# Kernel optimization log

Hardware: AMD Instinct MI355X
Metric: run time of the kernel (lower is better)

The kernel has to match this reference:

```python
import jax, jax.numpy as jnp
import numpy as np


def setup_inputs() -> dict:
    key0 = jax.random.key(0)
    kq, kk, kv, kl = jax.random.split(key0, 4)
    B, L, V, D = 2, 512, 64, 128
    N_CLUSTERS = 8
    return {
        "query": jax.random.normal(kq, (B, L, V, D), dtype=jnp.float32),
        "key": jax.random.normal(kk, (B, L, V, D), dtype=jnp.float32),
        "value": jax.random.normal(kv, (B, L, V, D), dtype=jnp.float32),
        "label_arr": jax.random.randint(kl, (B, L), 0, N_CLUSTERS, dtype=jnp.int64)
        if jax.config.jax_enable_x64
        else jax.random.randint(kl, (B, L), 0, N_CLUSTERS, dtype=jnp.int32),
    }


def reference(query, key, value, label_arr):
    # query/key/value: (b, l, v, d); label_arr: (b, l)
    b, l, v, d = query.shape
    scale = 1.0 / (d ** 0.5)  # self.scale defaults to 1/sqrt(d_model)

    # sum of key over the v (cluster-member) dimension -> (b, l, d)
    sum_tot_vec = key.sum(axis=2)

    # scores[b,i,k,j] = query[b,i,k,:] . sum_tot_vec[b,j,:]
    scores = jnp.einsum("bikd,bjd->bikj", query, sum_tot_vec)

    # label-based mask: positions attend only within the same cluster label
    label_mask = label_arr[:, :, None] == label_arr[:, None, :]  # (b, l, l)
    scores = jnp.where(label_mask[:, :, None, :], scores, -jnp.inf)

    # masked softmax over the last (j) axis; every row has >=1 valid entry (self)
    A = jax.nn.softmax(scale * scores, axis=-1)

    # V[b,i,k,d] = sum_j A[b,i,k,j] * value[b,j,k,d]
    out = jnp.einsum("bikj,bjkd->bikd", A, value)
    return out
```

## Files before the change

kernel.cpp:

```cpp
#include <hip/hip_runtime.h>
#include <math.h>

#define B_ 2
#define L_ 512
#define V_ 64
#define D_ 128
#define NC_ 8
#define NMAX 128
#define PSTR 136
#define SCALE 0.08838834764831845f

#define FB_THREADS 128
#define FB_IT 64
#define FB_JT 8
#define MAXIT (L_ / FB_IT)

typedef short s16x8 __attribute__((ext_vector_type(8)));
typedef float f32x4 __attribute__((ext_vector_type(4)));

__device__ __forceinline__ unsigned short f2bf(float x) {
  unsigned int u = __float_as_uint(x);
  u += 0x7FFFu + ((u >> 16) & 1u);
  return (unsigned short)(u >> 16);
}
__device__ __forceinline__ float bf2f(unsigned short h) {
  return __uint_as_float((unsigned int)h << 16);
}

__global__ __launch_bounds__(L_) void cluster_index_kernel(
    const int* __restrict__ label, int* __restrict__ counts, int* __restrict__ jlist) {
  int b = blockIdx.x;
  int tid = threadIdx.x;
  __shared__ int lab[L_];
  lab[tid] = label[b * L_ + tid];
  if (tid < NC_) counts[b * NC_ + tid] = 0;
  __syncthreads();
  int my = lab[tid];
  int rank = 0, cnt = 0;
  for (int j = 0; j < L_; ++j) {
    int e = (lab[j] == my) ? 1 : 0;
    cnt += e;
    if (j < tid) rank += e;
  }
  jlist[(b * NC_ + my) * L_ + rank] = tid;
  if (rank == 0) counts[b * NC_ + my] = cnt;
}

__global__ __launch_bounds__(256) void sumkey_kernel(
    const float* __restrict__ key, float* __restrict__ S,
    unsigned short* __restrict__ Sh, unsigned short* __restrict__ Sl) {
  int idx = blockIdx.x * 256 + threadIdx.x;
  int d4 = idx & 31;
  int bj = idx >> 5;
  const float4* kp = (const float4*)(key + (size_t)bj * V_ * D_) + d4;
  float4 s = make_float4(0.f, 0.f, 0.f, 0.f);
#pragma unroll 8
  for (int v = 0; v < V_; ++v) {
    float4 x = kp[v * 32];
    s.x += x.x; s.y += x.y; s.z += x.z; s.w += x.w;
  }
  *((float4*)S + idx) = s;
  unsigned short h0 = f2bf(s.x), h1 = f2bf(s.y), h2 = f2bf(s.z), h3 = f2bf(s.w);
  *((ushort4*)Sh + idx) = make_ushort4(h0, h1, h2, h3);
  *((ushort4*)Sl + idx) = make_ushort4(
      f2bf(s.x - bf2f(h0)), f2bf(s.y - bf2f(h1)),
      f2bf(s.z - bf2f(h2)), f2bf(s.w - bf2f(h3)));
}

__global__ __launch_bounds__(256, 2) void fused_attn_kernel(
    const float* __restrict__ q, const float* __restrict__ vg,
    const unsigned short* __restrict__ Sh, const unsigned short* __restrict__ Sl,
    const int* __restrict__ counts, const int* __restrict__ jlist,
    float* __restrict__ out) {
  int bid = blockIdx.x;
  int k = bid & (V_ - 1);
  int c = (bid >> 6) & (NC_ - 1);
  int b = bid >> 9;
  int bc = b * NC_ + c;
  int n = counts[bc];
  if (n == 0 || n > NMAX) return;
  int np32 = (n + 31) & ~31;
  int nt = np32 >> 4;
  int ktn = np32 >> 5;
  int mtn = (n + 15) >> 4;

  int tid = threadIdx.x;
  int w = tid >> 6;
  int l = tid & 63, lr = l & 15, lg = l >> 4;

  __shared__ int jl[NMAX];
  __shared__ __align__(16) unsigned short VTh[64][PSTR];
  __shared__ __align__(16) unsigned short VTl[64][PSTR];
  __shared__ __align__(16) unsigned short Pm[NMAX][PSTR];

  for (int j = tid; j < np32; j += 256) jl[j] = jlist[bc * L_ + min(j, n - 1)];
  __syncthreads();

  auto stage_vt = [&](int dbase) {
    int d4 = tid & 15, jj = tid >> 4;
    for (int j = jj; j < np32; j += 16) {
      float4 x = *(const float4*)(vg + ((size_t)(b * L_ + jl[j]) * V_ + k) * D_
                                  + dbase + d4 * 4);
      float xs[4] = {x.x, x.y, x.z, x.w};
#pragma unroll
      for (int e = 0; e < 4; ++e) {
        unsigned short h = f2bf(xs[e]);
        VTh[d4 * 4 + e][j] = h;
        VTl[d4 * 4 + e][j] = f2bf(xs[e] - bf2f(h));
      }
    }
  };

  auto pv_half = [&](int dbase) {
    for (int mt = w; mt < mtn; mt += 4) {
#pragma unroll
      for (int dt = 0; dt < 4; ++dt) {
        f32x4 o = {0.f, 0.f, 0.f, 0.f};
#pragma unroll
        for (int kt = 0; kt < 4; ++kt) {
          if (kt < ktn) {
            s16x8 pa = *(const s16x8*)&Pm[mt * 16 + lr][kt * 32 + lg * 8];
            s16x8 vh = *(const s16x8*)&VTh[dt * 16 + lr][kt * 32 + lg * 8];
            s16x8 vl = *(const s16x8*)&VTl[dt * 16 + lr][kt * 32 + lg * 8];
            o = __builtin_amdgcn_mfma_f32_16x16x32_bf16(pa, vh, o, 0, 0, 0);
            o = __builtin_amdgcn_mfma_f32_16x16x32_bf16(pa, vl, o, 0, 0, 0);
          }
        }
#pragma unroll
        for (int reg = 0; reg < 4; ++reg) {
          int i = mt * 16 + lg * 4 + reg;
          if (i < n)
            out[((size_t)(b * L_ + jl[i]) * V_ + k) * D_ + dbase + dt * 16 + lr]
                = o[reg];
        }
      }
    }
  };

  stage_vt(0);
  __syncthreads();

  for (int mt = w; mt < mtn; mt += 4) {
    const float* qb = q + ((size_t)(b * L_ + jl[mt * 16 + lr]) * V_ + k) * D_ + lg * 8;
    s16x8 Ah[4], Al[4];
#pragma unroll
    for (int kk = 0; kk < 4; ++kk) {
      float4 x0 = *(const float4*)(qb + kk * 32);
      float4 x1 = *(const float4*)(qb + kk * 32 + 4);
      float xs[8] = {x0.x, x0.y, x0.z, x0.w, x1.x, x1.y, x1.z, x1.w};
#pragma unroll
      for (int e = 0; e < 8; ++e) {
        unsigned short h = f2bf(xs[e]);
        Ah[kk][e] = (short)h;
        Al[kk][e] = (short)f2bf(xs[e] - bf2f(h));
      }
    }

    f32x4 acc[8];
#pragma unroll
    for (int jt = 0; jt < 8; ++jt) {
      if (jt < nt) {
        int jrow = jl[jt * 16 + lr];
        const unsigned short* sbh = Sh + (size_t)(b * L_ + jrow) * D_ + lg * 8;
        const unsigned short* sbl = Sl + (size_t)(b * L_ + jrow) * D_ + lg * 8;
        f32x4 a = {0.f, 0.f, 0.f, 0.f};
#pragma unroll
        for (int kk = 0; kk < 4; ++kk) {
          s16x8 bh = *(const s16x8*)(sbh + kk * 32);
          s16x8 bl = *(const s16x8*)(sbl + kk * 32);
          a = __builtin_amdgcn_mfma_f32_16x16x32_bf16(Ah[kk], bh, a, 0, 0, 0);
          a = __builtin_amdgcn_mfma_f32_16x16x32_bf16(Al[kk], bh, a, 0, 0, 0);
          a = __builtin_amdgcn_mfma_f32_16x16x32_bf16(Ah[kk], bl, a, 0, 0, 0);
        }
        acc[jt] = a;
      }
    }

#pragma unroll
    for (int reg = 0; reg < 4; ++reg) {
      float sv[8];
      float mx = -3.0e38f;
#pragma unroll
      for (int jt = 0; jt < 8; ++jt) {
        if (jt < nt) {
          float x = ((jt * 16 + lr) < n) ? acc[jt][reg] * SCALE : -3.0e38f;
          sv[jt] = x;
          mx = fmaxf(mx, x);
        }
      }
      mx = fmaxf(mx, __shfl_xor(mx, 1));
      mx = fmaxf(mx, __shfl_xor(mx, 2));
      mx = fmaxf(mx, __shfl_xor(mx, 4));
      mx = fmaxf(mx, __shfl_xor(mx, 8));
      float sum = 0.f;
#pragma unroll
      for (int jt = 0; jt < 8; ++jt) {
        if (jt < nt) {
          float p = __expf(sv[jt] - mx);
          p = ((jt * 16 + lr) < n) ? p : 0.f;
          sv[jt] = p;
          sum += p;
        }
      }
      sum += __shfl_xor(sum, 1);
      sum += __shfl_xor(sum, 2);
      sum += __shfl_xor(sum, 4);
      sum += __shfl_xor(sum, 8);
      float inv = 1.0f / sum;
      int prow = mt * 16 + lg * 4 + reg;
#pragma unroll
      for (int jt = 0; jt < 8; ++jt)
        if (jt < nt) Pm[prow][jt * 16 + lr] = f2bf(sv[jt] * inv);
    }
  }

  pv_half(0);
  __syncthreads();
  stage_vt(64);
  __syncthreads();
  pv_half(64);
}

__global__ __launch_bounds__(FB_THREADS, 2) void clustered_attn_kernel(
    const float* __restrict__ q, const float* __restrict__ value,
    const float* __restrict__ S, const int* __restrict__ counts,
    const int* __restrict__ jlist, float* __restrict__ out) {
  int bid = blockIdx.x;
  int k = bid & (V_ - 1);
  int c = (bid >> 6) & (NC_ - 1);
  int b = (bid >> 9) & (B_ - 1);
  int itile = bid >> 10;
  int bc = b * NC_ + c;
  int n = counts[bc];
  if (n <= NMAX) return;
  int it0 = itile * FB_IT;
  if (it0 >= n) return;

  int tid = threadIdx.x;
  int dh = tid & 7;
  int sl = tid >> 3;

  __shared__ int jl[L_];
  __shared__ float S_t[FB_JT][D_];
  __shared__ float V_t[FB_JT][D_];

  for (int j = tid; j < n; j += FB_THREADS) jl[j] = jlist[bc * L_ + j];
  __syncthreads();

  bool act[4];
  float4 q4[4][4];
#pragma unroll
  for (int r = 0; r < 4; ++r) {
    int row = it0 + sl + 16 * r;
    act[r] = row < n;
    int i = jl[act[r] ? row : it0];
    const float* qrow = q + (size_t)((b * L_ + i) * V_ + k) * D_;
#pragma unroll
    for (int t = 0; t < 4; ++t) q4[r][t] = *(const float4*)(qrow + (dh + 8 * t) * 4);
  }

  float4 acc4[4][4];
#pragma unroll
  for (int r = 0; r < 4; ++r)
#pragma unroll
    for (int t = 0; t < 4; ++t) acc4[r][t] = make_float4(0.f, 0.f, 0.f, 0.f);
  float m[4], lden[4];
#pragma unroll
  for (int r = 0; r < 4; ++r) { m[r] = -INFINITY; lden[r] = 0.f; }

  const float4* S_t4 = (const float4*)&S_t[0][0];
  const float4* V_t4 = (const float4*)&V_t[0][0];

  for (int jt0 = 0; jt0 < n; jt0 += FB_JT) {
    int jn = min(FB_JT, n - jt0);
    __syncthreads();
#pragma unroll
    for (int rep = 0; rep < 2; ++rep) {
      int idx = tid + rep * FB_THREADS;
      int jj = idx >> 5;
      int d4 = idx & 31;
      int j = jl[jt0 + min(jj, jn - 1)];
      size_t rowbase = (size_t)(b * L_ + j);
      ((float4*)&S_t[0][0])[idx] = *(const float4*)(S + rowbase * D_ + d4 * 4);
      ((float4*)&V_t[0][0])[idx] =
          *(const float4*)(value + (rowbase * V_ + k) * D_ + d4 * 4);
    }
    __syncthreads();

    float s[4][FB_JT];
#pragma unroll
    for (int r = 0; r < 4; ++r)
#pragma unroll
      for (int jj = 0; jj < FB_JT; ++jj) s[r][jj] = 0.f;
#pragma unroll
    for (int t = 0; t < 4; ++t) {
#pragma unroll
      for (int jj = 0; jj < FB_JT; ++jj) {
        float4 sv = S_t4[jj * 32 + dh + 8 * t];
#pragma unroll
        for (int r = 0; r < 4; ++r) {
          float4 qv = q4[r][t];
          s[r][jj] = fmaf(qv.x, sv.x,
                     fmaf(qv.y, sv.y, fmaf(qv.z, sv.z, fmaf(qv.w, sv.w, s[r][jj]))));
        }
      }
    }
#pragma unroll
    for (int r = 0; r < 4; ++r)
#pragma unroll
      for (int jj = 0; jj < FB_JT; ++jj) {
        float v = s[r][jj] + __shfl_xor(s[r][jj], 1);
        v += __shfl_xor(v, 2);
        v += __shfl_xor(v, 4);
        s[r][jj] = v * SCALE;
      }
#pragma unroll
    for (int r = 0; r < 4; ++r) {
      float mnew = m[r];
#pragma unroll
      for (int jj = 0; jj < FB_JT; ++jj)
        if (jj < jn) mnew = fmaxf(mnew, s[r][jj]);
      float f = __expf(m[r] - mnew);
      m[r] = mnew;
#pragma unroll
      for (int t = 0; t < 4; ++t) {
        acc4[r][t].x *= f; acc4[r][t].y *= f;
        acc4[r][t].z *= f; acc4[r][t].w *= f;
      }
      float sum = 0.f;
#pragma unroll
      for (int jj = 0; jj < FB_JT; ++jj) {
        float p = (jj < jn) ? __expf(s[r][jj] - mnew) : 0.f;
        s[r][jj] = p;
        sum += p;
      }
      lden[r] = lden[r] * f + sum;
    }
#pragma unroll
    for (int t = 0; t < 4; ++t) {
#pragma unroll
      for (int jj = 0; jj < FB_JT; ++jj) {
        float4 vv = V_t4[jj * 32 + dh + 8 * t];
#pragma unroll
        for (int r = 0; r < 4; ++r) {
          float p = s[r][jj];
          acc4[r][t].x = fmaf(p, vv.x, acc4[r][t].x);
          acc4[r][t].y = fmaf(p, vv.y, acc4[r][t].y);
          acc4[r][t].z = fmaf(p, vv.z, acc4[r][t].z);
          acc4[r][t].w = fmaf(p, vv.w, acc4[r][t].w);
        }
      }
    }
  }

#pragma unroll
  for (int r = 0; r < 4; ++r) {
    if (act[r]) {
      int i = jl[it0 + sl + 16 * r];
      float inv = 1.0f / lden[r];
      float* op = out + (size_t)((b * L_ + i) * V_ + k) * D_;
#pragma unroll
      for (int t = 0; t < 4; ++t) {
        float4 o;
        o.x = acc4[r][t].x * inv;
        o.y = acc4[r][t].y * inv;
        o.z = acc4[r][t].z * inv;
        o.w = acc4[r][t].w * inv;
        *(float4*)(op + (dh + 8 * t) * 4) = o;
      }
    }
  }
}

extern "C" void kernel_launch(void* const* d_in, const int* in_sizes, int n_in,
                              void* d_out, int out_size, void* d_ws, size_t ws_size,
                              hipStream_t stream) {
  const float* q = (const float*)d_in[0];
  const float* key = (const float*)d_in[1];
  const float* value = (const float*)d_in[2];
  const int* label = (const int*)d_in[3];
  float* out = (float*)d_out;

  char* w8 = (char*)d_ws;
  int* counts = (int*)(w8 + 0);
  int* jlist = (int*)(w8 + 256);
  float* S = (float*)(w8 + 33280);
  unsigned short* Sh = (unsigned short*)(w8 + 557568);
  unsigned short* Sl = (unsigned short*)(w8 + 819712);

  cluster_index_kernel<<<B_, L_, 0, stream>>>(label, counts, jlist);
  sumkey_kernel<<<(B_ * L_ * D_ / 4) / 256, 256, 0, stream>>>(key, S, Sh, Sl);
  fused_attn_kernel<<<B_ * NC_ * V_, 256, 0, stream>>>(
      q, value, Sh, Sl, counts, jlist, out);
  clustered_attn_kernel<<<B_ * NC_ * V_ * MAXIT, FB_THREADS, 0, stream>>>(
      q, value, S, counts, jlist, out);
}
```

Baseline: 202.5 us.

## Stream value chunks with online softmax and cluster-contiguous summed keys

The fused attention kernel now processes keys in 32-wide chunks with an online (flash-style) softmax. This shrinks shared memory so four blocks can fit per CU, and the grid is split into two query-row halves per (batch, cluster, head). The summed-key bf16 hi/lo arrays are written in cluster-sorted order using new position and base arrays, so score loads are contiguous instead of gathered. The sum-key kernel is reorganized to one block per row with a shared-memory reduction. The trade-off is that each value chunk is staged and converted redundantly by both half-blocks, and there are more barriers per chunk.

```diff
diff --git a/kernel.cpp b/kernel.cpp
--- a/kernel.cpp
+++ b/kernel.cpp
@@ -7,7 +7,7 @@
 #define D_ 128
 #define NC_ 8
 #define NMAX 128
-#define PSTR 136
+#define VSTR 40
 #define SCALE 0.08838834764831845f
 
 #define FB_THREADS 128
@@ -28,7 +28,8 @@
 }
 
 __global__ __launch_bounds__(L_) void cluster_index_kernel(
-    const int* __restrict__ label, int* __restrict__ counts, int* __restrict__ jlist) {
+    const int* __restrict__ label, int* __restrict__ counts,
+    int* __restrict__ jlist, int* __restrict__ posarr, int* __restrict__ bases) {
   int b = blockIdx.x;
   int tid = threadIdx.x;
   __shared__ int lab[L_];
@@ -36,113 +37,78 @@
   if (tid < NC_) counts[b * NC_ + tid] = 0;
   __syncthreads();
   int my = lab[tid];
-  int rank = 0, cnt = 0;
+  int rank = 0, cnt = 0, base = 0;
   for (int j = 0; j < L_; ++j) {
     int e = (lab[j] == my) ? 1 : 0;
     cnt += e;
     if (j < tid) rank += e;
+    if (lab[j] < my) base++;
   }
   jlist[(b * NC_ + my) * L_ + rank] = tid;
-  if (rank == 0) counts[b * NC_ + my] = cnt;
+  posarr[b * L_ + tid] = base + rank;
+  if (rank == 0) { counts[b * NC_ + my] = cnt; bases[b * NC_ + my] = base; }
 }
 
 __global__ __launch_bounds__(256) void sumkey_kernel(
-    const float* __restrict__ key, float* __restrict__ S,
-    unsigned short* __restrict__ Sh, unsigned short* __restrict__ Sl) {
-  int idx = blockIdx.x * 256 + threadIdx.x;
-  int d4 = idx & 31;
-  int bj = idx >> 5;
-  const float4* kp = (const float4*)(key + (size_t)bj * V_ * D_) + d4;
-  float4 s = make_float4(0.f, 0.f, 0.f, 0.f);
+    const float* __restrict__ key, const int* __restrict__ posarr,
+    float* __restrict__ S, unsigned short* __restrict__ Sch,
+    unsigned short* __restrict__ Scl) {
+  int bj = blockIdx.x;
+  int tid = threadIdx.x;
+  int d = tid & 127, vh = tid >> 7;
+  const float* kp = key + (size_t)bj * V_ * D_ + vh * 32 * D_ + d;
+  float s = 0.f;
 #pragma unroll 8
-  for (int v = 0; v < V_; ++v) {
-    float4 x = kp[v * 32];
-    s.x += x.x; s.y += x.y; s.z += x.z; s.w += x.w;
-  }
-  *((float4*)S + idx) = s;
-  unsigned short h0 = f2bf(s.x), h1 = f2bf(s.y), h2 = f2bf(s.z), h3 = f2bf(s.w);
-  *((ushort4*)Sh + idx) = make_ushort4(h0, h1, h2, h3);
-  *((ushort4*)Sl + idx) = make_ushort4(
-      f2bf(s.x - bf2f(h0)), f2bf(s.y - bf2f(h1)),
-      f2bf(s.z - bf2f(h2)), f2bf(s.w - bf2f(h3)));
-}
-
-__global__ __launch_bounds__(256, 2) void fused_attn_kernel(
+  for (int v = 0; v < 32; ++v) s += kp[v * D_];
+  __shared__ float buf[D_];
+  if (vh) buf[d] = s;
+  __syncthreads();
+  if (!vh) {
+    s += buf[d];
+    S[(size_t)bj * D_ + d] = s;
+    int b = bj >> 9;
+    int crow = b * L_ + posarr[bj];
+    unsigned short h = f2bf(s);
+    Sch[(size_t)crow * D_ + d] = h;
+    Scl[(size_t)crow * D_ + d] = f2bf(s - bf2f(h));
+  }
+}
+
+__global__ __launch_bounds__(256, 4) void fused_attn_kernel(
     const float* __restrict__ q, const float* __restrict__ vg,
-    const unsigned short* __restrict__ Sh, const unsigned short* __restrict__ Sl,
+    const unsigned short* __restrict__ Sch, const unsigned short* __restrict__ Scl,
     const int* __restrict__ counts, const int* __restrict__ jlist,
-    float* __restrict__ out) {
+    const int* __restrict__ bases, float* __restrict__ out) {
   int bid = blockIdx.x;
   int k = bid & (V_ - 1);
   int c = (bid >> 6) & (NC_ - 1);
-  int b = bid >> 9;
+  int b = (bid >> 9) & (B_ - 1);
+  int mhalf = bid >> 10;
   int bc = b * NC_ + c;
   int n = counts[bc];
-  if (n == 0 || n > NMAX) return;
-  int np32 = (n + 31) & ~31;
-  int nt = np32 >> 4;
-  int ktn = np32 >> 5;
+  if (n == 0 || n > NMAX || n <= mhalf * 64) return;
+  int nch = (n + 31) >> 5;
   int mtn = (n + 15) >> 4;
 
   int tid = threadIdx.x;
-  int w = tid >> 6;
-  int l = tid & 63, lr = l & 15, lg = l >> 4;
+  int w = tid >> 6, l = tid & 63, lr = l & 15, lg = l >> 4;
+  int mt = mhalf * 4 + w;
+  bool wact = mt < mtn;
 
   __shared__ int jl[NMAX];
-  __shared__ __align__(16) unsigned short VTh[64][PSTR];
-  __shared__ __align__(16) unsigned short VTl[64][PSTR];
-  __shared__ __align__(16) unsigned short Pm[NMAX][PSTR];
-
-  for (int j = tid; j < np32; j += 256) jl[j] = jlist[bc * L_ + min(j, n - 1)];
+  __shared__ __align__(16) unsigned short VTh[D_][VSTR];
+  __shared__ __align__(16) unsigned short VTl[D_][VSTR];
+  __shared__ __align__(16) unsigned short Pw[4][16][VSTR];
+
+  for (int j = tid; j < NMAX; j += 256) jl[j] = jlist[bc * L_ + min(j, n - 1)];
   __syncthreads();
 
-  auto stage_vt = [&](int dbase) {
-    int d4 = tid & 15, jj = tid >> 4;
-    for (int j = jj; j < np32; j += 16) {
-      float4 x = *(const float4*)(vg + ((size_t)(b * L_ + jl[j]) * V_ + k) * D_
-                                  + dbase + d4 * 4);
-      float xs[4] = {x.x, x.y, x.z, x.w};
-#pragma unroll
-      for (int e = 0; e < 4; ++e) {
-        unsigned short h = f2bf(xs[e]);
-        VTh[d4 * 4 + e][j] = h;
-        VTl[d4 * 4 + e][j] = f2bf(xs[e] - bf2f(h));
-      }
-    }
-  };
-
-  auto pv_half = [&](int dbase) {
-    for (int mt = w; mt < mtn; mt += 4) {
-#pragma unroll
-      for (int dt = 0; dt < 4; ++dt) {
-        f32x4 o = {0.f, 0.f, 0.f, 0.f};
-#pragma unroll
-        for (int kt = 0; kt < 4; ++kt) {
-          if (kt < ktn) {
-            s16x8 pa = *(const s16x8*)&Pm[mt * 16 + lr][kt * 32 + lg * 8];
-            s16x8 vh = *(const s16x8*)&VTh[dt * 16 + lr][kt * 32 + lg * 8];
-            s16x8 vl = *(const s16x8*)&VTl[dt * 16 + lr][kt * 32 + lg * 8];
-            o = __builtin_amdgcn_mfma_f32_16x16x32_bf16(pa, vh, o, 0, 0, 0);
-            o = __builtin_amdgcn_mfma_f32_16x16x32_bf16(pa, vl, o, 0, 0, 0);
-          }
-        }
-#pragma unroll
-        for (int reg = 0; reg < 4; ++reg) {
-          int i = mt * 16 + lg * 4 + reg;
-          if (i < n)
-            out[((size_t)(b * L_ + jl[i]) * V_ + k) * D_ + dbase + dt * 16 + lr]
-                = o[reg];
-        }
-      }
-    }
-  };
-
-  stage_vt(0);
-  __syncthreads();
-
-  for (int mt = w; mt < mtn; mt += 4) {
-    const float* qb = q + ((size_t)(b * L_ + jl[mt * 16 + lr]) * V_ + k) * D_ + lg * 8;
-    s16x8 Ah[4], Al[4];
+  int cb = b * L_ + bases[bc];
+
+  s16x8 Ah[4], Al[4];
+  if (wact) {
+    int iq = jl[min(mt * 16 + lr, n - 1)];
+    const float* qb = q + ((size_t)(b * L_ + iq) * V_ + k) * D_ + lg * 8;
 #pragma unroll
     for (int kk = 0; kk < 4; ++kk) {
       float4 x0 = *(const float4*)(qb + kk * 32);
@@ -155,14 +121,41 @@
         Al[kk][e] = (short)f2bf(xs[e] - bf2f(h));
       }
     }
-
-    f32x4 acc[8];
-#pragma unroll
-    for (int jt = 0; jt < 8; ++jt) {
-      if (jt < nt) {
-        int jrow = jl[jt * 16 + lr];
-        const unsigned short* sbh = Sh + (size_t)(b * L_ + jrow) * D_ + lg * 8;
-        const unsigned short* sbl = Sl + (size_t)(b * L_ + jrow) * D_ + lg * 8;
+  }
+
+  f32x4 aco[8];
+#pragma unroll
+  for (int dt = 0; dt < 8; ++dt) aco[dt] = (f32x4){0.f, 0.f, 0.f, 0.f};
+  float mrow[4], lrow[4];
+#pragma unroll
+  for (int r = 0; r < 4; ++r) { mrow[r] = -INFINITY; lrow[r] = 0.f; }
+
+  int d32 = tid & 31, jj8 = tid >> 5;
+
+  for (int ch = 0; ch < nch; ++ch) {
+    __syncthreads();
+#pragma unroll
+    for (int it = 0; it < 4; ++it) {
+      int jloc = jj8 + it * 8;
+      int jg = jl[min(ch * 32 + jloc, n - 1)];
+      float4 x = *(const float4*)(vg + ((size_t)(b * L_ + jg) * V_ + k) * D_ + d32 * 4);
+      float xs[4] = {x.x, x.y, x.z, x.w};
+#pragma unroll
+      for (int e = 0; e < 4; ++e) {
+        unsigned short h = f2bf(xs[e]);
+        VTh[d32 * 4 + e][jloc] = h;
+        VTl[d32 * 4 + e][jloc] = f2bf(xs[e] - bf2f(h));
+      }
+    }
+    __syncthreads();
+
+    if (wact) {
+      f32x4 aq0 = {0.f, 0.f, 0.f, 0.f}, aq1 = {0.f, 0.f, 0.f, 0.f};
+#pragma unroll
+      for (int jt = 0; jt < 2; ++jt) {
+        int jg = min(ch * 32 + jt * 16 + lr, n - 1);
+        const unsigned short* sbh = Sch + (size_t)(cb + jg) * D_ + lg * 8;
+        const unsigned short* sbl = Scl + (size_t)(cb + jg) * D_ + lg * 8;
         f32x4 a = {0.f, 0.f, 0.f, 0.f};
 #pragma unroll
         for (int kk = 0; kk < 4; ++kk) {
@@ -172,53 +165,56 @@
           a = __builtin_amdgcn_mfma_f32_16x16x32_bf16(Al[kk], bh, a, 0, 0, 0);
           a = __builtin_amdgcn_mfma_f32_16x16x32_bf16(Ah[kk], bl, a, 0, 0, 0);
         }
-        acc[jt] = a;
-      }
-    }
-
+        if (jt == 0) aq0 = a; else aq1 = a;
+      }
+#pragma unroll
+      for (int reg = 0; reg < 4; ++reg) {
+        float x0 = (ch * 32 + lr < n) ? aq0[reg] * SCALE : -3.0e38f;
+        float x1 = (ch * 32 + 16 + lr < n) ? aq1[reg] * SCALE : -3.0e38f;
+        float cm = fmaxf(x0, x1);
+        cm = fmaxf(cm, __shfl_xor(cm, 1));
+        cm = fmaxf(cm, __shfl_xor(cm, 2));
+        cm = fmaxf(cm, __shfl_xor(cm, 4));
+        cm = fmaxf(cm, __shfl_xor(cm, 8));
+        float mnew = fmaxf(mrow[reg], cm);
+        float f = __expf(mrow[reg] - mnew);
+        mrow[reg] = mnew;
+        float p0 = __expf(x0 - mnew);
+        float p1 = __expf(x1 - mnew);
+        float sum = p0 + p1;
+        sum += __shfl_xor(sum, 1);
+        sum += __shfl_xor(sum, 2);
+        sum += __shfl_xor(sum, 4);
+        sum += __shfl_xor(sum, 8);
+        lrow[reg] = lrow[reg] * f + sum;
+#pragma unroll
+        for (int dt = 0; dt < 8; ++dt) aco[dt][reg] *= f;
+        Pw[w][lg * 4 + reg][lr] = f2bf(p0);
+        Pw[w][lg * 4 + reg][16 + lr] = f2bf(p1);
+      }
+      s16x8 pa = *(const s16x8*)&Pw[w][lr][lg * 8];
+#pragma unroll
+      for (int dt = 0; dt < 8; ++dt) {
+        s16x8 vh = *(const s16x8*)&VTh[dt * 16 + lr][lg * 8];
+        s16x8 vl = *(const s16x8*)&VTl[dt * 16 + lr][lg * 8];
+        aco[dt] = __builtin_amdgcn_mfma_f32_16x16x32_bf16(pa, vh, aco[dt], 0, 0, 0);
+        aco[dt] = __builtin_amdgcn_mfma_f32_16x16x32_bf16(pa, vl, aco[dt], 0, 0, 0);
+      }
+    }
+  }
+
+  if (wact) {
 #pragma unroll
     for (int reg = 0; reg < 4; ++reg) {
-      float sv[8];
-      float mx = -3.0e38f;
-#pragma unroll
-      for (int jt = 0; jt < 8; ++jt) {
-        if (jt < nt) {
-          float x = ((jt * 16 + lr) < n) ? acc[jt][reg] * SCALE : -3.0e38f;
-          sv[jt] = x;
-          mx = fmaxf(mx, x);
-        }
-      }
-      mx = fmaxf(mx, __shfl_xor(mx, 1));
-      mx = fmaxf(mx, __shfl_xor(mx, 2));
-      mx = fmaxf(mx, __shfl_xor(mx, 4));
-      mx = fmaxf(mx, __shfl_xor(mx, 8));
-      float sum = 0.f;
-#pragma unroll
-      for (int jt = 0; jt < 8; ++jt) {
-        if (jt < nt) {
-          float p = __expf(sv[jt] - mx);
-          p = ((jt * 16 + lr) < n) ? p : 0.f;
-          sv[jt] = p;
-          sum += p;
-        }
-      }
-      sum += __shfl_xor(sum, 1);
-      sum += __shfl_xor(sum, 2);
-      sum += __shfl_xor(sum, 4);
-      sum += __shfl_xor(sum, 8);
-      float inv = 1.0f / sum;
-      int prow = mt * 16 + lg * 4 + reg;
-#pragma unroll
-      for (int jt = 0; jt < 8; ++jt)
-        if (jt < nt) Pm[prow][jt * 16 + lr] = f2bf(sv[jt] * inv);
-    }
-  }
-
-  pv_half(0);
-  __syncthreads();
-  stage_vt(64);
-  __syncthreads();
-  pv_half(64);
+      float inv = 1.0f / lrow[reg];
+      int ir = mt * 16 + lg * 4 + reg;
+      if (ir < n) {
+        float* op = out + ((size_t)(b * L_ + jl[ir]) * V_ + k) * D_ + lr;
+#pragma unroll
+        for (int dt = 0; dt < 8; ++dt) op[dt * 16] = aco[dt][reg] * inv;
+      }
+    }
+  }
 }
 
 __global__ __launch_bounds__(FB_THREADS, 2) void clustered_attn_kernel(
@@ -383,15 +379,17 @@
 
   char* w8 = (char*)d_ws;
   int* counts = (int*)(w8 + 0);
-  int* jlist = (int*)(w8 + 256);
-  float* S = (float*)(w8 + 33280);
-  unsigned short* Sh = (unsigned short*)(w8 + 557568);
-  unsigned short* Sl = (unsigned short*)(w8 + 819712);
-
-  cluster_index_kernel<<<B_, L_, 0, stream>>>(label, counts, jlist);
-  sumkey_kernel<<<(B_ * L_ * D_ / 4) / 256, 256, 0, stream>>>(key, S, Sh, Sl);
-  fused_attn_kernel<<<B_ * NC_ * V_, 256, 0, stream>>>(
-      q, value, Sh, Sl, counts, jlist, out);
+  int* bases = (int*)(w8 + 64);
+  int* posarr = (int*)(w8 + 256);
+  int* jlist = (int*)(w8 + 4352);
+  float* S = (float*)(w8 + 37120);
+  unsigned short* Sch = (unsigned short*)(w8 + 561408);
+  unsigned short* Scl = (unsigned short*)(w8 + 823552);
+
+  cluster_index_kernel<<<B_, L_, 0, stream>>>(label, counts, jlist, posarr, bases);
+  sumkey_kernel<<<B_ * L_, 256, 0, stream>>>(key, posarr, S, Sch, Scl);
+  fused_attn_kernel<<<B_ * NC_ * V_ * 2, 256, 0, stream>>>(
+      q, value, Sch, Scl, counts, jlist, bases, out);
   clustered_attn_kernel<<<B_ * NC_ * V_ * MAXIT, FB_THREADS, 0, stream>>>(
       q, value, S, counts, jlist, out);
 }
```

New measurement: 199.3 us. No clear change (-1.6%).
